# Kernel tuning notes

Measured on AMD Instinct MI355X. Metric: run time of the kernel, lower is better.

Reference implementation:

```python
import jax, jax.numpy as jnp
import numpy as np
from math import sqrt, pi

B, L, H, E = 16, 512, 8, 64
D = 64


def setup_inputs() -> dict:
    key = jax.random.key(0)
    k1, k2, k3, k4, k5 = jax.random.split(key, 5)
    queries = jax.random.normal(k1, (B, L, H, E), dtype=jnp.float32)
    keys = jax.random.normal(k2, (B, L, H, E), dtype=jnp.float32)
    values = jax.random.normal(k3, (B, L, H, D), dtype=jnp.float32)
    sigma = jax.random.normal(k4, (B, L, H), dtype=jnp.float32)
    head_gate_logit = jax.random.normal(k5, (H,), dtype=jnp.float32)
    # TriangularCausalMask: triu(ones, diagonal=1), broadcast over B,H
    attn_mask = jnp.triu(jnp.ones((L, L), dtype=bool), k=1)[None, None, :, :]
    attn_mask = jnp.broadcast_to(attn_mask, (B, 1, L, L))
    return {"queries": queries, "keys": keys, "values": values,
            "sigma": sigma, "head_gate_logit": head_gate_logit,
            "attn_mask": attn_mask}


def reference(queries, keys, values, sigma, head_gate_logit, attn_mask):
    Bq, Lq, Hq, Eq = queries.shape
    scale = 1.0 / sqrt(Eq)
    # scores: [B,H,L,S]
    scores = jnp.einsum('blhe,bshe->bhls', queries, keys)
    scores = jnp.where(attn_mask, -jnp.inf, scores)
    series = jax.nn.softmax(scale * scores, axis=-1)  # dropout p=0 -> identity

    # sigma: [B,L,H] -> [B,H,L]
    sig = jnp.transpose(sigma, (0, 2, 1))
    sig = jax.nn.sigmoid(sig * 5.0) + 1e-05
    sig = jnp.power(3.0, sig) - 1.0          # [B,H,L]
    sig = sig[..., None]                      # [B,H,L,1]

    i = jnp.arange(Lq, dtype=jnp.float32)
    dist = jnp.abs(i[:, None] - i[None, :])   # [L,L] |i-j|
    prior = (1.0 / (sqrt(2.0 * pi) * sig)) * jnp.exp(-(dist ** 2) / (2.0 * sig ** 2))
    prior_norm = prior / (jnp.sum(prior, axis=-1, keepdims=True) + 1e-08)

    gate = jax.nn.sigmoid(head_gate_logit).reshape(1, Hq, 1, 1)
    fused = gate * series + (1.0 - gate) * prior_norm
    fused = fused / (jnp.sum(fused, axis=-1, keepdims=True) + 1e-08)

    V = jnp.einsum('bhls,bshd->blhd', fused, values)
    return V
```

## Files before the change

kernel.cpp:

```cpp
#include <hip/hip_runtime.h>


#define B_ 16
#define L_ 512
#define H_ 8
#define KST 72
#define VST 72
#define WST 36

typedef __attribute__((ext_vector_type(8))) short bf16x8;
typedef __attribute__((ext_vector_type(4))) float f32x4;
union FR { bf16x8 v; unsigned u[4]; uint4 q4; };

static __device__ __forceinline__ unsigned fbits(float x){union{float f;unsigned u;}c;c.f=x;return c.u;}
static __device__ __forceinline__ float tvf(float x){union{unsigned u;float f;}c;c.u=fbits(x)&0xFFFF0000u;return c.f;}
static __device__ __forceinline__ unsigned pk2(float a,float b){return __builtin_amdgcn_perm(fbits(b),fbits(a),0x07060302u);}

__global__ __launch_bounds__(256,4) void anomaly_attn(
    const float* __restrict__ Q, const float* __restrict__ K,
    const float* __restrict__ V, const float* __restrict__ Sig,
    const float* __restrict__ Gate, float* __restrict__ Out)
{
  __shared__ unsigned short Klds[64*KST];
  __shared__ unsigned short Vlds[64*VST];
  __shared__ unsigned We[4][16][WST];

  const int tid=threadIdx.x, lane=tid&63, wid=tid>>6, q=lane>>4, c=lane&15;
  const int idx=blockIdx.x, bh=idx&127, t=idx>>7, h=bh&7, b=bh>>3;
  const int l0w = t*64 + wid*16;
  const size_t bh_off = ((size_t)b*L_*H_ + h)*64;
  const float* __restrict__ Qb=Q+bh_off;
  const float* __restrict__ Kb=K+bh_off;
  const float* __restrict__ Vb=V+bh_off;

  const int kr=tid>>2, kcb=tid&3, srp=tid>>3, scb=tid&7;
  const int swz = (c&3)<<3;

  bf16x8 qf[2];
  {
    const float* qrow = Qb + (size_t)(l0w+c)*512;
    #pragma unroll
    for (int ks=0; ks<2; ++ks) {
      const float4 a = *(const float4*)(qrow + ks*32 + q*8);
      const float4 d4 = *(const float4*)(qrow + ks*32 + q*8 + 4);
      FR f;
      f.u[0]=pk2(a.x,a.y);  f.u[1]=pk2(a.z,a.w);
      f.u[2]=pk2(d4.x,d4.y); f.u[3]=pk2(d4.z,d4.w);
      qf[ks]=f.v;
    }
  }

  const float sgv = Sig[((size_t)b*L_ + l0w + c)*H_ + h];
  float sg = 1.f/(1.f+__expf(-5.f*sgv)) + 1e-5f;
  sg = exp2f(sg*1.5849625007211562f) - 1.f;
  const float invs = 0.3989422804014327f/sg;
  const float i2s2 = (0.5f/(sg*sg))*1.44269504088896f;

  float eP=0.f, pP=0.f;
  f32x4 accA[4], accB[4];
  #pragma unroll
  for (int n=0;n<4;++n){accA[n]=(f32x4)0.f;accB[n]=(f32x4)0.f;}

  for (int tile=0; tile<8; ++tile) {
    const int s0=tile*64;
    const bool live = tile<=t, diag = tile==t;
    const int delta = s0 - l0w;
    const bool bk0 = (delta    >= -95) && (delta    <= 79);
    const bool bk1 = (delta+32 >= -95) && (delta+32 <= 79);
    const bool vneed = live || bk0 || bk1;
    __syncthreads();

    if (vneed) {
      const float* vp = Vb + (size_t)(s0+2*srp)*512 + scb*8;
      const float4 va0=((const float4*)vp)[0], va1=((const float4*)vp)[1];
      const float4 vb0=((const float4*)(vp+512))[0], vb1=((const float4*)(vp+512))[1];
      const float lo[8]={va0.x,va0.y,va0.z,va0.w,va1.x,va1.y,va1.z,va1.w};
      const float hi[8]={vb0.x,vb0.y,vb0.z,vb0.w,vb1.x,vb1.y,vb1.z,vb1.w};
      const int gp=(srp>>2)^scb, rpl=srp&3;
      #pragma unroll
      for (int i=0;i<8;++i){
        unsigned* pp=(unsigned*)&Vlds[(scb*8+i)*VST + (gp<<3)];
        pp[rpl]=pk2(lo[i],hi[i]);
      }
    }
    if (live) {
      const float* kp = Kb + (size_t)(s0+kr)*512 + kcb*16;
      const float4 ka=((const float4*)kp)[0], kb2=((const float4*)kp)[1];
      const float4 kc2=((const float4*)kp)[2], kd2=((const float4*)kp)[3];
      uint4 w0,w1;
      w0.x=pk2(ka.x,ka.y);  w0.y=pk2(ka.z,ka.w);
      w0.z=pk2(kb2.x,kb2.y); w0.w=pk2(kb2.z,kb2.w);
      w1.x=pk2(kc2.x,kc2.y); w1.y=pk2(kc2.z,kc2.w);
      w1.z=pk2(kd2.x,kd2.y); w1.w=pk2(kd2.z,kd2.w);
      uint4* dst=(uint4*)&Klds[kr*KST + kcb*16];
      dst[0]=w0; dst[1]=w1;
    }
    __syncthreads();

    int ks2max = -1;
    if (live) {
      const int ntmax = diag ? wid : 3;
      ks2max = diag ? (wid>>1) : 1;
      f32x4 sacc[4];
      #pragma unroll
      for (int nt=0;nt<4;++nt) if (nt<=ntmax) {
        f32x4 s=(f32x4)0.f;
        #pragma unroll
        for (int ks=0;ks<2;++ks){
          const bf16x8 kf=*(const bf16x8*)&Klds[(nt*16+c)*KST + ks*32 + q*8];
          s=__builtin_amdgcn_mfma_f32_16x16x32_bf16(kf,qf[ks],s,0,0,0);
        }
        sacc[nt]=s;
      }
      #pragma unroll
      for (int nt=0;nt<4;++nt) {
        if (nt<=ntmax) {
          float ev[4];
          #pragma unroll
          for (int r=0;r<4;++r) ev[r]=exp2f(sacc[nt][r]*0.180336880110323f);
          if (diag && nt==wid) {
            #pragma unroll
            for (int r=0;r<4;++r) if (4*q+r > c) ev[r]=0.f;
          }
          #pragma unroll
          for (int r=0;r<4;++r) eP += tvf(ev[r]);
          uint2 w; w.x=pk2(ev[0],ev[1]); w.y=pk2(ev[2],ev[3]);
          *(uint2*)&We[wid][c][(nt*8+2*q)^swz]=w;
        } else if (nt <= 2*ks2max+1) {
          uint2 z; z.x=0u; z.y=0u;
          *(uint2*)&We[wid][c][(nt*8+2*q)^swz]=z;
        }
      }
    }
    asm volatile("s_waitcnt lgkmcnt(0)" ::: "memory");

    FR ef[2], pf[2];
    #pragma unroll
    for (int k2=0;k2<2;++k2){
      if (k2<=ks2max) ef[k2].q4 = *(const uint4*)&We[wid][c][(k2*16+4*q)^swz];
      if (k2 ? bk1 : bk0) {
        float pv[8];
        #pragma unroll
        for (int j=0;j<8;++j){
          const float dd=(float)(c - k2*32 - q*8 - j - delta);
          pv[j]=invs*exp2f(-dd*dd*i2s2);
          pP += tvf(pv[j]);
        }
        pf[k2].u[0]=pk2(pv[0],pv[1]); pf[k2].u[1]=pk2(pv[2],pv[3]);
        pf[k2].u[2]=pk2(pv[4],pv[5]); pf[k2].u[3]=pk2(pv[6],pv[7]);
      }
    }
    #pragma unroll
    for (int nd=0;nd<4;++nd){
      const int d=nd*16+c, dg7=(d>>3)&7;
      #pragma unroll
      for (int k2=0;k2<2;++k2){
        const bool pb = k2 ? bk1 : bk0;
        if (k2<=ks2max || pb) {
          const int g2=((k2<<2)+q)^dg7;
          const bf16x8 vf=*(const bf16x8*)&Vlds[d*VST + (g2<<3)];
          if (k2<=ks2max) accA[nd]=__builtin_amdgcn_mfma_f32_16x16x32_bf16(vf,ef[k2].v,accA[nd],0,0,0);
          if (pb)         accB[nd]=__builtin_amdgcn_mfma_f32_16x16x32_bf16(vf,pf[k2].v,accB[nd],0,0,0);
        }
      }
    }
    asm volatile("s_waitcnt lgkmcnt(0)" ::: "memory");
  }

  eP += __shfl_xor(eP,16,64); eP += __shfl_xor(eP,32,64);
  pP += __shfl_xor(pP,16,64); pP += __shfl_xor(pP,32,64);
  float g=Gate[h]; g=1.f/(1.f+__expf(-g));
  const float cA=g/eP;
  const float cB=(1.f-g)/(pP+1e-8f);
  const float Sf=g+(1.f-g)*(pP/(pP+1e-8f));
  const float nf=1.f/(Sf+1e-8f);
  #pragma unroll
  for (int nd=0;nd<4;++nd){
    float4 o;
    o.x=(cA*accA[nd][0]+cB*accB[nd][0])*nf;
    o.y=(cA*accA[nd][1]+cB*accB[nd][1])*nf;
    o.z=(cA*accA[nd][2]+cB*accB[nd][2])*nf;
    o.w=(cA*accA[nd][3]+cB*accB[nd][3])*nf;
    *(float4*)&Out[bh_off + (size_t)(l0w+c)*512 + nd*16 + 4*q] = o;
  }
}

extern "C" void kernel_launch(void* const* d_in, const int* in_sizes, int n_in,
                              void* d_out, int out_size, void* d_ws, size_t ws_size,
                              hipStream_t stream) {
    const float* Q    = (const float*)d_in[0];
    const float* K    = (const float*)d_in[1];
    const float* V    = (const float*)d_in[2];
    const float* Sig  = (const float*)d_in[3];
    const float* Gate = (const float*)d_in[4];
    float* Out = (float*)d_out;

    dim3 grid(8 * B_ * H_);
    anomaly_attn<<<grid, 256, 0, stream>>>(Q, K, V, Sig, Gate, Out);
}
```

Measured before the change: 124.0 us.

## Prefetch next tile's K and V into registers during current tile compute

Global loads of the K and V tiles move out of the store phase. The first tile is loaded before the loop, and each iteration issues the loads for tile+1 right after writing the current tile to LDS. Global memory latency can then overlap with the MFMA and exp work of the current tile instead of stalling right after the barrier. The cost is 16 extra live float registers per thread, which could pressure the 4-blocks-per-CU launch bound.

```diff
diff --git a/kernel.cpp b/kernel.cpp
--- a/kernel.cpp
+++ b/kernel.cpp
@@ -35,6 +35,16 @@
 
   const int kr=tid>>2, kcb=tid&3, srp=tid>>3, scb=tid&7;
   const int swz = (c&3)<<3;
+
+  const float* __restrict__ vbase = Vb + (size_t)(2*srp)*512 + scb*8;
+  const float* __restrict__ kbase = Kb + (size_t)kr*512 + kcb*16;
+
+  float4 sva0,sva1,svb0,svb1;
+  float4 ska,skb,skc,skd;
+  sva0=((const float4*)vbase)[0];       sva1=((const float4*)vbase)[1];
+  svb0=((const float4*)(vbase+512))[0]; svb1=((const float4*)(vbase+512))[1];
+  ska=((const float4*)kbase)[0]; skb=((const float4*)kbase)[1];
+  skc=((const float4*)kbase)[2]; skd=((const float4*)kbase)[3];
 
   bf16x8 qf[2];
   {
@@ -71,11 +81,8 @@
     __syncthreads();
 
     if (vneed) {
-      const float* vp = Vb + (size_t)(s0+2*srp)*512 + scb*8;
-      const float4 va0=((const float4*)vp)[0], va1=((const float4*)vp)[1];
-      const float4 vb0=((const float4*)(vp+512))[0], vb1=((const float4*)(vp+512))[1];
-      const float lo[8]={va0.x,va0.y,va0.z,va0.w,va1.x,va1.y,va1.z,va1.w};
-      const float hi[8]={vb0.x,vb0.y,vb0.z,vb0.w,vb1.x,vb1.y,vb1.z,vb1.w};
+      const float lo[8]={sva0.x,sva0.y,sva0.z,sva0.w,sva1.x,sva1.y,sva1.z,sva1.w};
+      const float hi[8]={svb0.x,svb0.y,svb0.z,svb0.w,svb1.x,svb1.y,svb1.z,svb1.w};
       const int gp=(srp>>2)^scb, rpl=srp&3;
       #pragma unroll
       for (int i=0;i<8;++i){
@@ -84,16 +91,29 @@
       }
     }
     if (live) {
-      const float* kp = Kb + (size_t)(s0+kr)*512 + kcb*16;
-      const float4 ka=((const float4*)kp)[0], kb2=((const float4*)kp)[1];
-      const float4 kc2=((const float4*)kp)[2], kd2=((const float4*)kp)[3];
       uint4 w0,w1;
-      w0.x=pk2(ka.x,ka.y);  w0.y=pk2(ka.z,ka.w);
-      w0.z=pk2(kb2.x,kb2.y); w0.w=pk2(kb2.z,kb2.w);
-      w1.x=pk2(kc2.x,kc2.y); w1.y=pk2(kc2.z,kc2.w);
-      w1.z=pk2(kd2.x,kd2.y); w1.w=pk2(kd2.z,kd2.w);
+      w0.x=pk2(ska.x,ska.y);  w0.y=pk2(ska.z,ska.w);
+      w0.z=pk2(skb.x,skb.y);  w0.w=pk2(skb.z,skb.w);
+      w1.x=pk2(skc.x,skc.y);  w1.y=pk2(skc.z,skc.w);
+      w1.z=pk2(skd.x,skd.y);  w1.w=pk2(skd.z,skd.w);
       uint4* dst=(uint4*)&Klds[kr*KST + kcb*16];
       dst[0]=w0; dst[1]=w1;
+    }
+    if (tile<7) {
+      const int s1=s0+64, d1=s1-l0w;
+      const bool live1 = (tile+1)<=t;
+      const bool b0n = (d1    >= -95) && (d1    <= 79);
+      const bool b1n = (d1+32 >= -95) && (d1+32 <= 79);
+      const float* vp = vbase + (size_t)s1*512;
+      const float* kp = kbase + (size_t)s1*512;
+      if (live1 || b0n || b1n) {
+        sva0=((const float4*)vp)[0];       sva1=((const float4*)vp)[1];
+        svb0=((const float4*)(vp+512))[0]; svb1=((const float4*)(vp+512))[1];
+      }
+      if (live1) {
+        ska=((const float4*)kp)[0]; skb=((const float4*)kp)[1];
+        skc=((const float4*)kp)[2]; skd=((const float4*)kp)[3];
+      }
     }
     __syncthreads();
 
```

After: 159.4 us. +28.5%, slower.
